# Performance work log

Hardware: AMD Instinct MI355X
Metric: run time of the kernel (lower is better)

Reference implementation:

```python
import jax, jax.numpy as jnp
import numpy as np

DIM = 1024
N_SRC = 4096
N_TGT = 4096


def setup_inputs() -> dict:
    key = jax.random.key(0)
    ks = jax.random.split(key, 7)
    scale = 1.0 / np.sqrt(DIM)
    return {
        "source": jax.random.normal(ks[0], (N_SRC, DIM), dtype=jnp.float32),
        "target": jax.random.normal(ks[1], (N_TGT, DIM), dtype=jnp.float32),
        "W_src": jax.random.uniform(ks[2], (DIM, DIM), minval=-scale, maxval=scale, dtype=jnp.float32),
        "b_src": jax.random.uniform(ks[3], (DIM,), minval=-scale, maxval=scale, dtype=jnp.float32),
        "W_tgt": jax.random.uniform(ks[4], (DIM, DIM), minval=-scale, maxval=scale, dtype=jnp.float32),
        "b_tgt": jax.random.uniform(ks[5], (DIM,), minval=-scale, maxval=scale, dtype=jnp.float32),
        "temperature": jnp.array(1.0, dtype=jnp.float32),
    }


def reference(source, target, W_src, b_src, W_tgt, b_tgt, temperature):
    # Linear projections (torch Linear: x @ W.T + b)
    sp = source @ W_src.T + b_src            # [N, d]
    tp = target @ W_tgt.T + b_tgt            # [M, d]
    sq_s = jnp.sum(sp * sp, axis=-1, keepdims=True)   # [N, 1]
    sq_t = jnp.sum(tp * tp, axis=-1)                  # [M]
    d2 = sq_s + sq_t[None, :] - 2.0 * (sp @ tp.T)     # [N, M]
    cost = jnp.sqrt(jnp.maximum(d2, 0.0))
    # Softmin-style kernel, row-normalized over target entries
    K = jnp.exp(-cost / temperature)
    K = K / jnp.sum(K, axis=1, keepdims=True)
    aligned_source = K @ target                       # [N, d]
    return aligned_source, K
```

## Files before the change

kernel.cpp:

```cpp
#include <hip/hip_runtime.h>
#include <stdint.h>

#define DIM  1024
#define NSRC 4096
#define NTGT 4096

typedef __bf16 bf16_t;
typedef bf16_t bf16x8 __attribute__((ext_vector_type(8)));
typedef float  fx4    __attribute__((ext_vector_type(4)));

static __device__ __forceinline__ unsigned short f2bf(float f) {
  union { float f; uint32_t u; } v; v.f = f;
  return (unsigned short)((v.u + 0x7FFFu + ((v.u >> 16) & 1u)) >> 16);
}
static __device__ __forceinline__ float bf2f(unsigned short h) {
  union { uint32_t u; float f; } v; v.u = ((uint32_t)h) << 16;
  return v.f;
}

static __device__ __forceinline__ void gl_lds16(const unsigned short* g, unsigned short* l) {
  __builtin_amdgcn_global_load_lds(
      (__attribute__((address_space(1))) const void*)g,
      (__attribute__((address_space(3))) void*)l, 16, 0, 0);
}

typedef const __attribute__((address_space(3))) unsigned short* lds3p;

template <int IMM>
static __device__ __forceinline__ bf16x8 dsr128(lds3p p) {
  bf16x8 r;
  asm volatile("ds_read_b128 %0, %1 offset:%2" : "=v"(r) : "v"(p), "n"(IMM));
  return r;
}


__global__ void k_convert_all(const float* __restrict__ s, const float* __restrict__ t,
                              const float* __restrict__ w0, const float* __restrict__ w1,
                              unsigned short* __restrict__ sb, unsigned short* __restrict__ tb,
                              unsigned short* __restrict__ wb0, unsigned short* __restrict__ wb1) {
  int b = blockIdx.x;
  const float* in; unsigned short* out; int idx;
  if (b < 4096)      { in = s;  out = sb;  idx = b * 256 + threadIdx.x; }
  else if (b < 8192) { in = t;  out = tb;  idx = (b - 4096) * 256 + threadIdx.x; }
  else if (b < 9216) { in = w0; out = wb0; idx = (b - 8192) * 256 + threadIdx.x; }
  else               { in = w1; out = wb1; idx = (b - 9216) * 256 + threadIdx.x; }
  float4 v = ((const float4*)in)[idx];
  ushort4 o;
  o.x = f2bf(v.x); o.y = f2bf(v.y); o.z = f2bf(v.z); o.w = f2bf(v.w);
  ((ushort4*)out)[idx] = o;
}

__global__ void k_transpose_bf16(const float* __restrict__ in, unsigned short* __restrict__ out,
                                 int R, int C) {
  __shared__ unsigned short tile[32][33];
  int c0 = blockIdx.x * 32, r0 = blockIdx.y * 32;
  int tx = threadIdx.x, ty = threadIdx.y;
  for (int i = ty; i < 32; i += 8) {
    int row = r0 + i;
    int p = row & 63;
    int tr = (row & ~63) | ((p >> 2) | ((p & 3) << 4));
    tile[i][tx] = f2bf(in[(size_t)tr * C + c0 + tx]);
  }
  __syncthreads();
  for (int i = ty; i < 32; i += 8)
    out[(size_t)(c0 + i) * R + r0 + tx] = tile[tx][i];
}

__global__ void k_finalize_aligned(const float* __restrict__ P, float* __restrict__ aligned,
                                   const float* __restrict__ rs) {
  const int b = blockIdx.x;
  const int lane = threadIdx.x & 63, w = threadIdx.x >> 6;
  const int src = ((lane & 15) << 2) | (lane >> 4);
  const size_t stride = (size_t)NSRC * DIM;
#pragma unroll
  for (int it = 0; it < 4; ++it) {
    int idx = b * 16 + w * 4 + it;
    size_t base = (size_t)idx * 64;
    float r = 1.0f / rs[idx >> 4];
    float v = (P[base + lane] + P[base + stride + lane] +
               P[base + 2 * stride + lane] + P[base + 3 * stride + lane]) * r;
    aligned[base + lane] = __shfl(v, src, 64);
  }
}

__global__ void k_finalize_K(const unsigned short* __restrict__ Eb, float* __restrict__ Kf,
                             const float* __restrict__ rs) {
  const int b = blockIdx.x;
  const int lane = threadIdx.x & 63, w = threadIdx.x >> 6;
  const int src = ((lane & 15) << 2) | (lane >> 4);
#pragma unroll
  for (int it = 0; it < 8; ++it) {
    int idx = b * 32 + w * 8 + it;
    size_t base = (size_t)idx * 64;
    float r = 1.0f / rs[idx >> 6];
    float v = bf2f(Eb[base + lane]) * r;
    Kf[base + lane] = __shfl(v, src, 64);
  }
}

template <int EPI, int LDK>
__global__ void __launch_bounds__(512, 2)
k_tile256(const unsigned short* __restrict__ A0, const unsigned short* __restrict__ B0,
          const unsigned short* __restrict__ A1, const unsigned short* __restrict__ B1,
          const float* __restrict__ bias0, const float* __restrict__ bias1,
          unsigned short* __restrict__ Cb0, unsigned short* __restrict__ Cb1,
          unsigned short* __restrict__ Eb, float* __restrict__ Cf,
          const float* __restrict__ sqs, const float* __restrict__ sqt,
          const float* __restrict__ tempPtr,
          float* __restrict__ red0, float* __restrict__ red1) {
  __shared__ unsigned short ldsA[32768];
  __shared__ unsigned short ldsB[32768];

  const unsigned short* A = A0;
  const unsigned short* B = B0;
  const float* bias = bias0;
  unsigned short* Cb = Cb0;
  float* red = red0;
  if constexpr (EPI == 0) {
    if (blockIdx.z) { A = A1; B = B1; bias = bias1; Cb = Cb1; red = red1; }
  }
  if constexpr (EPI == 3) { A += blockIdx.z * 1024; B += blockIdx.z * 1024; }

  int nbx = blockIdx.x, nby = blockIdx.y;
  {
    const int nx = gridDim.x, n = gridDim.x * gridDim.y;
    const int id = nby * nx + nbx;
    const int q = n >> 3;
    const int s = (id & 7) * q + (id >> 3);
    nbx = s % nx; nby = s / nx;
  }

  const int tid = threadIdx.x;
  const int lane = tid & 63, w = tid >> 6;
  const int wm = w >> 2, wn = w & 3;
  const int fr = lane & 15, kq = lane >> 4;
  const int m0 = nby * 256, n0 = nbx * 256;

  const int rin = lane >> 2;
  const int cs  = ((lane & 3) * 8) ^ ((lane >> 5) ? 16 : 0);
  const size_t aoff0 = (size_t)(m0 + w * 16 + rin) * LDK + cs;
  const size_t aoff1 = (size_t)(m0 + (8 + w) * 16 + rin) * LDK + cs;
  const size_t boff0 = (size_t)(n0 + w * 16 + rin) * LDK + cs;
  const size_t boff1 = (size_t)(n0 + (8 + w) * 16 + rin) * LDK + cs;

  const int roA = fr * 32 + ((kq * 8) ^ ((fr & 8) ? 16 : 0));
  const lds3p baseA = (lds3p)ldsA + wm * 4096 + roA;
  const lds3p baseB = (lds3p)ldsB + wn * 2048 + roA;

#define STAGE_A(buf, ksb, kk) do { \
    gl_lds16(A + aoff0 + (kk) + (ksb) * 32, ldsA + (buf) * 16384 + (ksb) * 8192 + w * 512); \
    gl_lds16(A + aoff1 + (kk) + (ksb) * 32, ldsA + (buf) * 16384 + (ksb) * 8192 + (8 + w) * 512); \
  } while (0)
#define STAGE_B(buf, ksb, kk) do { \
    gl_lds16(B + boff0 + (kk) + (ksb) * 32, ldsB + (buf) * 16384 + (ksb) * 8192 + w * 512); \
    gl_lds16(B + boff1 + (kk) + (ksb) * 32, ldsB + (buf) * 16384 + (ksb) * 8192 + (8 + w) * 512); \
  } while (0)

  const fx4 fz = {0.f, 0.f, 0.f, 0.f};
  fx4 acc[8][4];
#pragma unroll
  for (int i = 0; i < 8; ++i)
#pragma unroll
    for (int j = 0; j < 4; ++j) acc[i][j] = fz;

  bf16x8 a[8], b0v, b1v, b2v, b3v;

#define LDA1(buf, ks, i) a[i] = dsr128<(buf) * 32768 + (ks) * 16384 + (i) * 1024>(baseA)
#define LDA8(buf, ks) do { \
    LDA1(buf, ks, 0); LDA1(buf, ks, 1); LDA1(buf, ks, 2); LDA1(buf, ks, 3); \
    LDA1(buf, ks, 4); LDA1(buf, ks, 5); LDA1(buf, ks, 6); LDA1(buf, ks, 7); \
  } while (0)
#define LDB2(buf, ks, jh, r0, r1) do { \
    r0 = dsr128<(buf) * 32768 + (ks) * 16384 + (jh) * 2048>(baseB); \
    r1 = dsr128<(buf) * 32768 + (ks) * 16384 + (jh) * 2048 + 1024>(baseB); \
  } while (0)
#define MFMA16(jh, r0, r1) do { _Pragma("unroll") \
    for (int i = 0; i < 8; ++i) { \
      acc[i][(jh) * 2]     = __builtin_amdgcn_mfma_f32_16x16x32_bf16(a[i], r0, acc[i][(jh) * 2], 0, 0, 0); \
      acc[i][(jh) * 2 + 1] = __builtin_amdgcn_mfma_f32_16x16x32_bf16(a[i], r1, acc[i][(jh) * 2 + 1], 0, 0, 0); \
    } } while (0)
#define SB0()   __builtin_amdgcn_sched_barrier(0)
#define BARS()  do { SB0(); __builtin_amdgcn_s_barrier(); SB0(); } while (0)
#define LGKM2() do { asm volatile("s_waitcnt lgkmcnt(2)" ::: "memory"); SB0(); } while (0)
#define LGKM0() do { asm volatile("s_waitcnt lgkmcnt(0)" ::: "memory"); SB0(); } while (0)
#define VM4()   asm volatile("s_waitcnt vmcnt(4)" ::: "memory")

#define PHASE(buf, ks, sb, sk, kk) do { \
    LDB2(buf, ks, 0, b0v, b1v); LDA8(buf, ks); LDB2(buf, ks, 1, b2v, b3v); \
    STAGE_A(sb, sk, kk); STAGE_B(sb, sk, kk); \
    BARS(); LGKM2(); \
    __builtin_amdgcn_s_setprio(1); \
    MFMA16(0, b0v, b1v); \
    LGKM0(); \
    MFMA16(1, b2v, b3v); \
    __builtin_amdgcn_s_setprio(0); \
  } while (0)

  STAGE_A(0, 0, 0);  STAGE_B(0, 0, 0);  STAGE_A(0, 1, 0);  STAGE_B(0, 1, 0);
  STAGE_A(1, 0, 64); STAGE_B(1, 0, 64);
  VM4();
  BARS();

#pragma unroll 1
  for (int it = 0; it < 8; ++it) {
    const int kk1 = it * 128 + 64;
    const int kk2 = (it * 128 + 128) & 1023;
    const int kk3 = (it * 128 + 192) & 1023;
    PHASE(0, 0, 1, 1, kk1);
    BARS();
    PHASE(0, 1, 0, 0, kk2);
    VM4();
    BARS();
    PHASE(1, 0, 0, 1, kk2);
    BARS();
    PHASE(1, 1, 1, 0, kk3);
    VM4();
    BARS();
  }
  asm volatile("s_waitcnt vmcnt(0)" ::: "memory");
  __syncthreads();

  const int gcol0 = n0 + wn * 64 + fr;
  const int scol  = n0 + wn * 64 + fr * 4;

  if constexpr (EPI == 0) {
#pragma unroll
    for (int i = 0; i < 8; ++i)
#pragma unroll
      for (int r = 0; r < 4; ++r) {
        const int gm = m0 + wm * 128 + i * 16 + kq * 4 + r;
        float racc = 0.f;
        ushort4 o; unsigned short* op = (unsigned short*)&o;
#pragma unroll
        for (int j = 0; j < 4; ++j) {
          float e = acc[i][j][r] + bias[gcol0 + j * 16];
          unsigned short eb = f2bf(e);
          op[j] = eb;
          float ev = bf2f(eb);
          racc += ev * ev;
        }
        *(ushort4*)(Cb + (size_t)gm * DIM + scol) = o;
        racc += __shfl_xor(racc, 1, 64);
        racc += __shfl_xor(racc, 2, 64);
        racc += __shfl_xor(racc, 4, 64);
        racc += __shfl_xor(racc, 8, 64);
        if (fr == 0) atomicAdd(&red[gm], racc);
      }
  } else if constexpr (EPI == 1) {
    const float invT = 1.0f / tempPtr[0];
#pragma unroll
    for (int i = 0; i < 8; ++i)
#pragma unroll
      for (int r = 0; r < 4; ++r) {
        const int gm = m0 + wm * 128 + i * 16 + kq * 4 + r;
        const float si = sqs[gm];
        float racc = 0.f;
        ushort4 o; unsigned short* op = (unsigned short*)&o;
#pragma unroll
        for (int j = 0; j < 4; ++j) {
          float d2 = si + sqt[gcol0 + j * 16] - 2.0f * acc[i][j][r];
          float c = sqrtf(fmaxf(d2, 0.0f));
          unsigned short eb = f2bf(__expf(-c * invT));
          op[j] = eb;
          racc += bf2f(eb);
        }
        *(ushort4*)(Eb + (size_t)gm * NTGT + scol) = o;
        racc += __shfl_xor(racc, 1, 64);
        racc += __shfl_xor(racc, 2, 64);
        racc += __shfl_xor(racc, 4, 64);
        racc += __shfl_xor(racc, 8, 64);
        if (fr == 0) atomicAdd(&red[gm], racc);
      }
  } else {
    float* Pz = Cf + (size_t)blockIdx.z * NSRC * DIM;
#pragma unroll
    for (int i = 0; i < 8; ++i)
#pragma unroll
      for (int r = 0; r < 4; ++r) {
        const int gm = m0 + wm * 128 + i * 16 + kq * 4 + r;
        float4 v = make_float4(acc[i][0][r], acc[i][1][r], acc[i][2][r], acc[i][3][r]);
        *(float4*)(Pz + (size_t)gm * DIM + scol) = v;
      }
  }
#undef STAGE_A
#undef STAGE_B
#undef LDA1
#undef LDA8
#undef LDB2
#undef MFMA16
#undef PHASE
#undef SB0
#undef BARS
#undef LGKM2
#undef LGKM0
#undef VM4
}

extern "C" void kernel_launch(void* const* d_in, const int* in_sizes, int n_in,
                              void* d_out, int out_size, void* d_ws, size_t ws_size,
                              hipStream_t stream) {
  const float* source = (const float*)d_in[0];
  const float* target = (const float*)d_in[1];
  const float* W_src  = (const float*)d_in[2];
  const float* b_src  = (const float*)d_in[3];
  const float* W_tgt  = (const float*)d_in[4];
  const float* b_tgt  = (const float*)d_in[5];
  const float* temp   = (const float*)d_in[6];

  float* out     = (float*)d_out;
  float* aligned = out;
  float* Kout    = out + (size_t)NSRC * DIM;
  float* parts   = Kout;

  char* ws = (char*)d_ws;
  unsigned short* src_b  = (unsigned short*)(ws + 0);
  unsigned short* tgt_b  = (unsigned short*)(ws + 8388608);
  unsigned short* Wsrc_b = (unsigned short*)(ws + 16777216);
  unsigned short* Wtgt_b = (unsigned short*)(ws + 18874368);
  unsigned short* sp_b   = (unsigned short*)(ws + 20971520);
  unsigned short* tp_b   = (unsigned short*)(ws + 29360128);
  unsigned short* tgtT_b = (unsigned short*)(ws + 37748736);
  unsigned short* E_b    = (unsigned short*)(ws + 46137344);
  float* sq_s  = (float*)(ws + 79691776);
  float* sq_t  = (float*)(ws + 79708160);
  float* rsums = (float*)(ws + 79724544);

  hipMemsetAsync(sq_s, 0, 3 * NSRC * sizeof(float), stream);

  k_convert_all<<<10240, 256, 0, stream>>>(source, target, W_src, W_tgt,
                                           src_b, tgt_b, Wsrc_b, Wtgt_b);
  k_transpose_bf16<<<dim3(DIM / 32, NTGT / 32), dim3(32, 8), 0, stream>>>(target, tgtT_b, NTGT, DIM);

  k_tile256<0, DIM><<<dim3(DIM / 256, NSRC / 256, 2), 512, 0, stream>>>(
      src_b, Wsrc_b, tgt_b, Wtgt_b, b_src, b_tgt, sp_b, tp_b,
      nullptr, nullptr, nullptr, nullptr, nullptr, sq_s, sq_t);

  k_tile256<1, DIM><<<dim3(NTGT / 256, NSRC / 256, 1), 512, 0, stream>>>(
      sp_b, tp_b, nullptr, nullptr, nullptr, nullptr, nullptr, nullptr,
      E_b, nullptr, sq_s, sq_t, temp, rsums, nullptr);

  k_tile256<3, NTGT><<<dim3(DIM / 256, NSRC / 256, 4), 512, 0, stream>>>(
      E_b, tgtT_b, nullptr, nullptr, nullptr, nullptr, nullptr, nullptr,
      nullptr, parts, nullptr, nullptr, nullptr, nullptr, nullptr);

  k_finalize_aligned<<<4096, 256, 0, stream>>>(parts, aligned, rsums);
  k_finalize_K<<<8192, 256, 0, stream>>>(E_b, Kout, rsums);
}
```

Baseline: 276.7 us.

## Restructure GEMM mainloop to 64-wide K tiles with XOR-swizzled LDS layout

Replaces the four-phase 32-wide K sub-block pipeline with a double-buffered loop over 64-wide K tiles. Each wave now reads all 24 A/B fragments from LDS, waits for them, then issues the next tile's global-to-LDS copies and runs 64 MFMAs. The LDS layout moves to 64-element rows with an 8-way XOR swizzle to avoid bank conflicts. This cuts the number of barriers and waitcnts per K step. In exchange it holds more fragment registers and loses the overlap between LDS reads and MFMAs within a phase.

Result: no change. 277.0 us (+0.1%).

```diff
diff --git a/kernel.cpp b/kernel.cpp
--- a/kernel.cpp
+++ b/kernel.cpp
@@ -136,24 +136,26 @@
   const int fr = lane & 15, kq = lane >> 4;
   const int m0 = nby * 256, n0 = nbx * 256;
 
-  const int rin = lane >> 2;
-  const int cs  = ((lane & 3) * 8) ^ ((lane >> 5) ? 16 : 0);
-  const size_t aoff0 = (size_t)(m0 + w * 16 + rin) * LDK + cs;
-  const size_t aoff1 = (size_t)(m0 + (8 + w) * 16 + rin) * LDK + cs;
-  const size_t boff0 = (size_t)(n0 + w * 16 + rin) * LDK + cs;
-  const size_t boff1 = (size_t)(n0 + (8 + w) * 16 + rin) * LDK + cs;
-
-  const int roA = fr * 32 + ((kq * 8) ^ ((fr & 8) ? 16 : 0));
-  const lds3p baseA = (lds3p)ldsA + wm * 4096 + roA;
-  const lds3p baseB = (lds3p)ldsB + wn * 2048 + roA;
-
-#define STAGE_A(buf, ksb, kk) do { \
-    gl_lds16(A + aoff0 + (kk) + (ksb) * 32, ldsA + (buf) * 16384 + (ksb) * 8192 + w * 512); \
-    gl_lds16(A + aoff1 + (kk) + (ksb) * 32, ldsA + (buf) * 16384 + (ksb) * 8192 + (8 + w) * 512); \
-  } while (0)
-#define STAGE_B(buf, ksb, kk) do { \
-    gl_lds16(B + boff0 + (kk) + (ksb) * 32, ldsB + (buf) * 16384 + (ksb) * 8192 + w * 512); \
-    gl_lds16(B + boff1 + (kk) + (ksb) * 32, ldsB + (buf) * 16384 + (ksb) * 8192 + (8 + w) * 512); \
+  const int rg = lane >> 3;
+  const int sk = ((lane & 7) ^ rg) * 8;
+  const size_t aS = (size_t)(m0 + w * 8 + rg) * LDK + sk;
+  const size_t bS = (size_t)(n0 + w * 8 + rg) * LDK + sk;
+
+  const int eA = fr & 7;
+  const lds3p baseA0 = (lds3p)ldsA + (wm * 128 + fr) * 64 + ((kq ^ eA) * 8);
+  const lds3p baseA1 = (lds3p)ldsA + (wm * 128 + fr) * 64 + (((4 + kq) ^ eA) * 8);
+  const lds3p baseB0 = (lds3p)ldsB + (wn * 64 + fr) * 64 + ((kq ^ eA) * 8);
+  const lds3p baseB1 = (lds3p)ldsB + (wn * 64 + fr) * 64 + (((4 + kq) ^ eA) * 8);
+
+#define STAGE(buf, tk) do { \
+    gl_lds16(A + aS + (size_t)(tk),                 ldsA + (buf) * 16384 + w * 512); \
+    gl_lds16(A + aS + 64 * (size_t)LDK + (tk),      ldsA + (buf) * 16384 + 4096 + w * 512); \
+    gl_lds16(A + aS + 128 * (size_t)LDK + (tk),     ldsA + (buf) * 16384 + 8192 + w * 512); \
+    gl_lds16(A + aS + 192 * (size_t)LDK + (tk),     ldsA + (buf) * 16384 + 12288 + w * 512); \
+    gl_lds16(B + bS + (size_t)(tk),                 ldsB + (buf) * 16384 + w * 512); \
+    gl_lds16(B + bS + 64 * (size_t)LDK + (tk),      ldsB + (buf) * 16384 + 4096 + w * 512); \
+    gl_lds16(B + bS + 128 * (size_t)LDK + (tk),     ldsB + (buf) * 16384 + 8192 + w * 512); \
+    gl_lds16(B + bS + 192 * (size_t)LDK + (tk),     ldsB + (buf) * 16384 + 12288 + w * 512); \
   } while (0)
 
   const fx4 fz = {0.f, 0.f, 0.f, 0.f};
@@ -163,62 +165,77 @@
 #pragma unroll
     for (int j = 0; j < 4; ++j) acc[i][j] = fz;
 
-  bf16x8 a[8], b0v, b1v, b2v, b3v;
-
-#define LDA1(buf, ks, i) a[i] = dsr128<(buf) * 32768 + (ks) * 16384 + (i) * 1024>(baseA)
-#define LDA8(buf, ks) do { \
-    LDA1(buf, ks, 0); LDA1(buf, ks, 1); LDA1(buf, ks, 2); LDA1(buf, ks, 3); \
-    LDA1(buf, ks, 4); LDA1(buf, ks, 5); LDA1(buf, ks, 6); LDA1(buf, ks, 7); \
+  bf16x8 a[8][2], b[4][2];
+
+#define RD24(buf) do { \
+    a[0][0] = dsr128<(buf) * 32768 +     0>(baseA0); \
+    a[1][0] = dsr128<(buf) * 32768 +  2048>(baseA0); \
+    a[2][0] = dsr128<(buf) * 32768 +  4096>(baseA0); \
+    a[3][0] = dsr128<(buf) * 32768 +  6144>(baseA0); \
+    a[4][0] = dsr128<(buf) * 32768 +  8192>(baseA0); \
+    a[5][0] = dsr128<(buf) * 32768 + 10240>(baseA0); \
+    a[6][0] = dsr128<(buf) * 32768 + 12288>(baseA0); \
+    a[7][0] = dsr128<(buf) * 32768 + 14336>(baseA0); \
+    a[0][1] = dsr128<(buf) * 32768 +     0>(baseA1); \
+    a[1][1] = dsr128<(buf) * 32768 +  2048>(baseA1); \
+    a[2][1] = dsr128<(buf) * 32768 +  4096>(baseA1); \
+    a[3][1] = dsr128<(buf) * 32768 +  6144>(baseA1); \
+    a[4][1] = dsr128<(buf) * 32768 +  8192>(baseA1); \
+    a[5][1] = dsr128<(buf) * 32768 + 10240>(baseA1); \
+    a[6][1] = dsr128<(buf) * 32768 + 12288>(baseA1); \
+    a[7][1] = dsr128<(buf) * 32768 + 14336>(baseA1); \
+    b[0][0] = dsr128<(buf) * 32768 +     0>(baseB0); \
+    b[1][0] = dsr128<(buf) * 32768 +  2048>(baseB0); \
+    b[2][0] = dsr128<(buf) * 32768 +  4096>(baseB0); \
+    b[3][0] = dsr128<(buf) * 32768 +  6144>(baseB0); \
+    b[0][1] = dsr128<(buf) * 32768 +     0>(baseB1); \
+    b[1][1] = dsr128<(buf) * 32768 +  2048>(baseB1); \
+    b[2][1] = dsr128<(buf) * 32768 +  4096>(baseB1); \
+    b[3][1] = dsr128<(buf) * 32768 +  6144>(baseB1); \
   } while (0)
-#define LDB2(buf, ks, jh, r0, r1) do { \
-    r0 = dsr128<(buf) * 32768 + (ks) * 16384 + (jh) * 2048>(baseB); \
-    r1 = dsr128<(buf) * 32768 + (ks) * 16384 + (jh) * 2048 + 1024>(baseB); \
-  } while (0)
-#define MFMA16(jh, r0, r1) do { _Pragma("unroll") \
-    for (int i = 0; i < 8; ++i) { \
-      acc[i][(jh) * 2]     = __builtin_amdgcn_mfma_f32_16x16x32_bf16(a[i], r0, acc[i][(jh) * 2], 0, 0, 0); \
-      acc[i][(jh) * 2 + 1] = __builtin_amdgcn_mfma_f32_16x16x32_bf16(a[i], r1, acc[i][(jh) * 2 + 1], 0, 0, 0); \
-    } } while (0)
+
+#define MFMA64() do { _Pragma("unroll") \
+    for (int i = 0; i < 8; ++i) { _Pragma("unroll") \
+      for (int j = 0; j < 4; ++j) { \
+        acc[i][j] = __builtin_amdgcn_mfma_f32_16x16x32_bf16(a[i][0], b[j][0], acc[i][j], 0, 0, 0); \
+        acc[i][j] = __builtin_amdgcn_mfma_f32_16x16x32_bf16(a[i][1], b[j][1], acc[i][j], 0, 0, 0); \
+      } } } while (0)
+
 #define SB0()   __builtin_amdgcn_sched_barrier(0)
 #define BARS()  do { SB0(); __builtin_amdgcn_s_barrier(); SB0(); } while (0)
-#define LGKM2() do { asm volatile("s_waitcnt lgkmcnt(2)" ::: "memory"); SB0(); } while (0)
 #define LGKM0() do { asm volatile("s_waitcnt lgkmcnt(0)" ::: "memory"); SB0(); } while (0)
-#define VM4()   asm volatile("s_waitcnt vmcnt(4)" ::: "memory")
-
-#define PHASE(buf, ks, sb, sk, kk) do { \
-    LDB2(buf, ks, 0, b0v, b1v); LDA8(buf, ks); LDB2(buf, ks, 1, b2v, b3v); \
-    STAGE_A(sb, sk, kk); STAGE_B(sb, sk, kk); \
-    BARS(); LGKM2(); \
-    __builtin_amdgcn_s_setprio(1); \
-    MFMA16(0, b0v, b1v); \
+#define VM8()   do { asm volatile("s_waitcnt vmcnt(8)" ::: "memory"); SB0(); } while (0)
+#define VM0()   do { asm volatile("s_waitcnt vmcnt(0)" ::: "memory"); SB0(); } while (0)
+
+#define PH_MAIN(buf, tk2) do { \
+    RD24(buf); \
     LGKM0(); \
-    MFMA16(1, b2v, b3v); \
-    __builtin_amdgcn_s_setprio(0); \
+    BARS(); \
+    STAGE(buf, tk2); SB0(); \
+    __builtin_amdgcn_s_setprio(1); MFMA64(); __builtin_amdgcn_s_setprio(0); \
+    VM8(); \
+    BARS(); \
   } while (0)
 
-  STAGE_A(0, 0, 0);  STAGE_B(0, 0, 0);  STAGE_A(0, 1, 0);  STAGE_B(0, 1, 0);
-  STAGE_A(1, 0, 64); STAGE_B(1, 0, 64);
-  VM4();
+  STAGE(0, 0);
+  STAGE(1, 64);
+  VM8();
   BARS();
 
 #pragma unroll 1
-  for (int it = 0; it < 8; ++it) {
-    const int kk1 = it * 128 + 64;
-    const int kk2 = (it * 128 + 128) & 1023;
-    const int kk3 = (it * 128 + 192) & 1023;
-    PHASE(0, 0, 1, 1, kk1);
-    BARS();
-    PHASE(0, 1, 0, 0, kk2);
-    VM4();
-    BARS();
-    PHASE(1, 0, 0, 1, kk2);
-    BARS();
-    PHASE(1, 1, 1, 0, kk3);
-    VM4();
-    BARS();
-  }
-  asm volatile("s_waitcnt vmcnt(0)" ::: "memory");
-  __syncthreads();
+  for (int it = 0; it < 7; ++it) {
+    PH_MAIN(0, it * 128 + 128);
+    PH_MAIN(1, it * 128 + 192);
+  }
+  RD24(0);
+  LGKM0();
+  BARS();
+  __builtin_amdgcn_s_setprio(1); MFMA64(); __builtin_amdgcn_s_setprio(0);
+  VM0();
+  BARS();
+  RD24(1);
+  LGKM0();
+  __builtin_amdgcn_s_setprio(1); MFMA64(); __builtin_amdgcn_s_setprio(0);
 
   const int gcol0 = n0 + wn * 64 + fr;
   const int scol  = n0 + wn * 64 + fr * 4;
@@ -282,18 +299,15 @@
         *(float4*)(Pz + (size_t)gm * DIM + scol) = v;
       }
   }
-#undef STAGE_A
-#undef STAGE_B
-#undef LDA1
-#undef LDA8
-#undef LDB2
-#undef MFMA16
-#undef PHASE
+#undef STAGE
+#undef RD24
+#undef MFMA64
+#undef PH_MAIN
 #undef SB0
 #undef BARS
-#undef LGKM2
 #undef LGKM0
-#undef VM4
+#undef VM8
+#undef VM0
 }
 
 extern "C" void kernel_launch(void* const* d_in, const int* in_sizes, int n_in,
```
